# Kernel tuning notes

Measured on AMD Instinct MI355X. Metric: run time of the kernel, lower is better.

Reference implementation:

```python
import jax, jax.numpy as jnp
import numpy as np

NUM_TOURS = 200   # fixed segment count (original: tour_index.max()+1)
EPS = 1e-5        # torch InstanceNorm1d default eps


def setup_inputs() -> dict:
    key = jax.random.key(0)
    ks = jax.random.split(key, 9)
    B, P, D = 64, 2000, 128
    embeddings = jax.random.normal(ks[0], (B, P + 1, D), jnp.float32)
    tour_index = jax.random.randint(ks[1], (B, P), 0, NUM_TOURS, dtype=jnp.int32)
    # tour_combiner: Linear(2D -> D); feedforward: Linear(D -> D); stored as (in, out)
    W1 = jax.random.normal(ks[2], (2 * D, D), jnp.float32) / np.sqrt(2 * D)
    b1 = jax.random.normal(ks[3], (D,), jnp.float32) * 0.01
    W2 = jax.random.normal(ks[4], (D, D), jnp.float32) / np.sqrt(D)
    b2 = jax.random.normal(ks[5], (D,), jnp.float32) * 0.01
    # InstanceNorm1d affine params (per channel)
    gamma = 1.0 + 0.1 * jax.random.normal(ks[6], (D,), jnp.float32)
    beta = 0.1 * jax.random.normal(ks[7], (D,), jnp.float32)
    return {
        "batch_size": B, "num_customers": P,
        "tour_index": tour_index, "embeddings": embeddings,
        "W1": W1, "b1": b1, "W2": W2, "b2": b2,
        "gamma": gamma, "beta": beta,
    }


def reference(batch_size, num_customers, tour_index, embeddings, W1, b1, W2, b2, gamma, beta):
    B, P = batch_size, num_customers
    D = embeddings.shape[-1]
    cust = embeddings[:, 1:]                                  # (B, P, D)
    # tour-level segment sum (scatter_add over tour ids, per batch)
    flat_idx = (tour_index + jnp.arange(B, dtype=tour_index.dtype)[:, None] * NUM_TOURS).reshape(-1)
    tour_emb = jax.ops.segment_sum(cust.reshape(B * P, D), flat_idx,
                                   num_segments=B * NUM_TOURS).reshape(B, NUM_TOURS, D)
    # gather tour embedding back to each customer
    cust_tour = jnp.take_along_axis(tour_emb, tour_index[:, :, None], axis=1)  # (B, P, D)
    # concat -> linear -> relu -> linear
    combined = jnp.concatenate([cust, cust_tour], axis=-1)    # (B, P, 2D)
    h = jax.nn.relu(combined @ W1 + b1)
    h = h @ W2 + b2
    # residual + instance norm over the customer axis, per channel
    added = cust + h
    mean = jnp.mean(added, axis=1, keepdims=True)
    var = jnp.var(added, axis=1, keepdims=True)
    normed = (added - mean) * jax.lax.rsqrt(var + EPS) * gamma + beta
    return jnp.concatenate([embeddings[:, :1], normed], axis=1)
```

## Files before the change

kernel.cpp:

```cpp
#include <hip/hip_runtime.h>
#include <stdint.h>

typedef unsigned short u16;
typedef __attribute__((ext_vector_type(8))) short short8;
typedef __attribute__((ext_vector_type(4))) float floatx4;

constexpr int B_ = 64, P_ = 2000, D_ = 128, T_ = 200;

__device__ __forceinline__ u16 f2bf(float f) {
  union { float f; uint32_t u; } v; v.f = f;
  return (u16)((v.u + 0x7fffu + ((v.u >> 16) & 1u)) >> 16);
}

__global__ __launch_bounds__(256) void k_pre(
    const int* __restrict__ tidx, int* __restrict__ list,
    int* __restrict__ goff, int* __restrict__ gcnt,
    const float* __restrict__ W1, const float* __restrict__ W2,
    u16* __restrict__ w1f, u16* __restrict__ w2f, float* __restrict__ ssum) {
  __shared__ int tix[P_];
  __shared__ int cnt[256], scan[256], cur[256];
  const int bid = blockIdx.x, tid = threadIdx.x;

  if (bid >= 64) {
    if (bid < 128) {
      ssum[(bid - 64) * 256 + tid] = 0.f;
      return;
    }
    int t = (bid - 128) * 256 + tid;
    if (t >= 6144) return;
    const float* W = (t < 4096) ? W1 : W2;
    u16* dst = (t < 4096) ? w1f : w2f;
    int fid = (t < 4096) ? t : t - 4096;
    int lane = fid & 63;
    int nt = (fid >> 6) & 7;
    int ks = fid >> 9;
    int quad = lane >> 4, c = lane & 15;
    int k0 = ks * 32 + quad * 8;
#pragma unroll
    for (int j = 0; j < 8; ++j)
      dst[(size_t)fid * 8 + j] = f2bf(W[(k0 + j) * D_ + nt * 16 + c]);
    return;
  }

  const int b = bid;
  cnt[tid] = 0;
  for (int i = tid; i < P_; i += 256) tix[i] = tidx[b * P_ + i];
  __syncthreads();
  for (int i = tid; i < P_; i += 256) atomicAdd(&cnt[tix[i]], 1);
  __syncthreads();
  scan[tid] = cnt[tid];
  __syncthreads();
  for (int s = 1; s < 256; s <<= 1) {
    int v = (tid >= s) ? scan[tid - s] : 0;
    __syncthreads();
    scan[tid] += v;
    __syncthreads();
  }
  int excl = scan[tid] - cnt[tid];
  if (tid < T_) {
    goff[b * T_ + tid] = excl;
    gcnt[b * T_ + tid] = cnt[tid];
  }
  cur[tid] = excl;
  __syncthreads();
  for (int i = tid; i < P_; i += 256) {
    int slot = atomicAdd(&cur[tix[i]], 1);
    list[b * P_ + slot] = i;
  }
}

__global__ __launch_bounds__(256) void k_gather(const float* __restrict__ emb,
                                                const int* __restrict__ list,
                                                const int* __restrict__ goff,
                                                const int* __restrict__ gcnt,
                                                u16* __restrict__ tourb) {
  const int tid = threadIdx.x;
  const int lane = tid & 63, wv = tid >> 6;
  const int seg = blockIdx.x * 4 + wv;
  const int b = seg / T_;
  const int off = goff[seg], cn = gcnt[seg];
  const int* lstb = list + b * P_;
  const float* eb = emb + ((size_t)(b * 2001 + 1)) * D_ + lane * 2;
  float sx = 0.f, sy = 0.f;
  for (int i = 0; i < cn; i += 8) {
    int pr[8];
#pragma unroll
    for (int j = 0; j < 8; ++j)
      if (i + j < cn) pr[j] = lstb[off + i + j];
    float2 v[8];
#pragma unroll
    for (int j = 0; j < 8; ++j)
      if (i + j < cn) v[j] = *(const float2*)(eb + (size_t)pr[j] * D_);
#pragma unroll
    for (int j = 0; j < 8; ++j)
      if (i + j < cn) { sx += v[j].x; sy += v[j].y; }
  }
  uint32_t pk = (uint32_t)f2bf(sx) | ((uint32_t)f2bf(sy) << 16);
  ((uint32_t*)(tourb + (size_t)seg * D_))[lane] = pk;
}

__global__ __launch_bounds__(256, 8) void k_mlp(
    const int* __restrict__ tidx, const float* __restrict__ emb,
    const u16* __restrict__ tourb,
    const u16* __restrict__ w1f, const u16* __restrict__ w2f,
    const float* __restrict__ b1, const float* __restrict__ b2,
    float* __restrict__ ssum, float* __restrict__ ssq,
    float* __restrict__ out) {
  __shared__ u16 hbuf[32 * 136];
  __shared__ float red[2][2][128];
  const int tid = threadIdx.x;
  const int w = tid >> 6, lane = tid & 63, quad = lane >> 4, c = lane & 15;
  const int wr = w >> 1, wc = w & 1;
  const int base = blockIdx.x * 32;
  const int r0 = wr * 16;

  for (int i = tid; i < 512; i += 256) ((float*)red)[i] = 0.f;

  const int blo = base / P_;
  const int bhi = (base + 31) / P_;
  const bool straddle = (blo != bhi);
  const int bsplit = bhi * P_;

  const int m0 = base + r0 + c;
  const int ab = m0 / P_, ap = m0 - ab * P_;
  const float* arow = emb + ((size_t)(ab * 2001 + 1 + ap)) * D_;
  const u16* trow = tourb + ((size_t)(ab * T_ + tidx[m0])) * D_;

  float bias1[4], bias2[4];
#pragma unroll
  for (int ntl = 0; ntl < 4; ++ntl) {
    bias1[ntl] = b1[(wc * 4 + ntl) * 16 + c];
    bias2[ntl] = b2[(wc * 4 + ntl) * 16 + c];
  }

  floatx4 acc[4];
#pragma unroll
  for (int ntl = 0; ntl < 4; ++ntl) acc[ntl] = (floatx4)0.f;

#pragma unroll
  for (int ks = 0; ks < 8; ++ks) {
    short8 a;
    if (ks < 4) {
      const float* src = arow + ks * 32 + quad * 8;
      floatx4 x0 = *(const floatx4*)src;
      floatx4 x1 = *(const floatx4*)(src + 4);
#pragma unroll
      for (int j = 0; j < 4; ++j) {
        a[j]     = (short)f2bf(x0[j]);
        a[4 + j] = (short)f2bf(x1[j]);
      }
    } else {
      a = *(const short8*)(trow + (ks - 4) * 32 + quad * 8);
    }
#pragma unroll
    for (int ntl = 0; ntl < 4; ++ntl) {
      int nt = wc * 4 + ntl;
      short8 bf = *(const short8*)(w1f + ((size_t)((ks * 8 + nt) * 64 + lane)) * 8);
      acc[ntl] = __builtin_amdgcn_mfma_f32_16x16x32_bf16(a, bf, acc[ntl], 0, 0, 0);
    }
  }

#pragma unroll
  for (int ntl = 0; ntl < 4; ++ntl)
#pragma unroll
    for (int r = 0; r < 4; ++r) {
      int row = r0 + quad * 4 + r;
      float v = acc[ntl][r] + bias1[ntl];
      hbuf[row * 136 + wc * 64 + ntl * 16 + c] = f2bf(v > 0.f ? v : 0.f);
    }
  __syncthreads();

  floatx4 acc2[4];
#pragma unroll
  for (int ntl = 0; ntl < 4; ++ntl) acc2[ntl] = (floatx4)0.f;

#pragma unroll
  for (int ks = 0; ks < 4; ++ks) {
    short8 a = *(const short8*)(&hbuf[(r0 + c) * 136 + ks * 32 + quad * 8]);
#pragma unroll
    for (int ntl = 0; ntl < 4; ++ntl) {
      int nt = wc * 4 + ntl;
      short8 bf = *(const short8*)(w2f + ((size_t)((ks * 8 + nt) * 64 + lane)) * 8);
      acc2[ntl] = __builtin_amdgcn_mfma_f32_16x16x32_bf16(a, bf, acc2[ntl], 0, 0, 0);
    }
  }

  float s[4], q[4];
#pragma unroll
  for (int ntl = 0; ntl < 4; ++ntl) { s[ntl] = 0.f; q[ntl] = 0.f; }
#pragma unroll
  for (int ntl = 0; ntl < 4; ++ntl)
#pragma unroll
    for (int r = 0; r < 4; ++r) {
      int row = r0 + quad * 4 + r;
      int m = base + row;
      int b = m / P_, p = m - b * P_;
      int col = wc * 64 + ntl * 16 + c;
      size_t gaddr = ((size_t)(b * 2001 + 1 + p)) * D_ + col;
      float v = emb[gaddr] + (acc2[ntl][r] + bias2[ntl]);
      out[gaddr] = v;
      if (!straddle || m < bsplit) {
        s[ntl] += v; q[ntl] += v * v;
      } else {
        atomicAdd(&red[1][0][col], v);
        atomicAdd(&red[1][1][col], v * v);
      }
    }
#pragma unroll
  for (int ntl = 0; ntl < 4; ++ntl) {
    s[ntl] += __shfl_xor(s[ntl], 16);
    s[ntl] += __shfl_xor(s[ntl], 32);
    q[ntl] += __shfl_xor(q[ntl], 16);
    q[ntl] += __shfl_xor(q[ntl], 32);
  }
  if (quad == 0) {
#pragma unroll
    for (int ntl = 0; ntl < 4; ++ntl) {
      int col = wc * 64 + ntl * 16 + c;
      atomicAdd(&red[0][0][col], s[ntl]);
      atomicAdd(&red[0][1][col], q[ntl]);
    }
  }
  __syncthreads();
  if (tid < 128) {
    atomicAdd(&ssum[blo * D_ + tid], red[0][0][tid]);
    if (straddle) atomicAdd(&ssum[bhi * D_ + tid], red[1][0][tid]);
  } else {
    int col = tid - 128;
    atomicAdd(&ssq[blo * D_ + col], red[0][1][col]);
    if (straddle) atomicAdd(&ssq[bhi * D_ + col], red[1][1][col]);
  }
}

__global__ __launch_bounds__(256) void k_out(
    const float* __restrict__ emb,
    const float* __restrict__ ssum, const float* __restrict__ ssq,
    const float* __restrict__ gamma, const float* __restrict__ beta,
    float* __restrict__ out) {
  size_t i = ((size_t)blockIdx.x * 256 + threadIdx.x) * 8;
  int row = (int)(i >> 7), col = (int)(i & 127);
  int b = row / 2001, r = row - b * 2001;
  if (r == 0) {
    *(floatx4*)(out + i)     = *(const floatx4*)(emb + i);
    *(floatx4*)(out + i + 4) = *(const floatx4*)(emb + i + 4);
  } else {
    floatx4 a0 = *(const floatx4*)(out + i);
    floatx4 a1 = *(const floatx4*)(out + i + 4);
    int cc = b * D_ + col;
    floatx4 su0 = *(const floatx4*)(ssum + cc);
    floatx4 su1 = *(const floatx4*)(ssum + cc + 4);
    floatx4 sq0 = *(const floatx4*)(ssq + cc);
    floatx4 sq1 = *(const floatx4*)(ssq + cc + 4);
    floatx4 g0  = *(const floatx4*)(gamma + col);
    floatx4 g1  = *(const floatx4*)(gamma + col + 4);
    floatx4 be0 = *(const floatx4*)(beta + col);
    floatx4 be1 = *(const floatx4*)(beta + col + 4);
    constexpr float invP = 1.f / P_;
#pragma unroll
    for (int j = 0; j < 4; ++j) {
      float mean = su0[j] * invP;
      float var  = sq0[j] * invP - mean * mean;
      float sc   = rsqrtf(var + 1e-5f) * g0[j];
      a0[j] = a0[j] * sc + (be0[j] - mean * sc);
      float mean1 = su1[j] * invP;
      float var1  = sq1[j] * invP - mean1 * mean1;
      float sc1   = rsqrtf(var1 + 1e-5f) * g1[j];
      a1[j] = a1[j] * sc1 + (be1[j] - mean1 * sc1);
    }
    *(floatx4*)(out + i)     = a0;
    *(floatx4*)(out + i + 4) = a1;
  }
}

extern "C" void kernel_launch(void* const* d_in, const int* in_sizes, int n_in,
                              void* d_out, int out_size, void* d_ws, size_t ws_size,
                              hipStream_t stream) {
  const int*   tour_index = (const int*)d_in[2];
  const float* emb   = (const float*)d_in[3];
  const float* W1    = (const float*)d_in[4];
  const float* b1    = (const float*)d_in[5];
  const float* W2    = (const float*)d_in[6];
  const float* b2    = (const float*)d_in[7];
  const float* gamma = (const float*)d_in[8];
  const float* beta  = (const float*)d_in[9];
  float* out = (float*)d_out;
  char* ws = (char*)d_ws;

  u16*   w1f   = (u16*)(ws);
  u16*   w2f   = (u16*)(ws + 65536);
  float* ssum  = (float*)(ws + 98304);
  float* ssq   = ssum + B_ * D_;
  u16*   tourb = (u16*)(ws + 229376);
  int*   list  = (int*)(ws + 3506176);
  int*   goff  = (int*)(ws + 4018176);
  int*   gcnt  = (int*)(ws + 4069376);

  hipLaunchKernelGGL(k_pre,    dim3(152),  dim3(256), 0, stream,
                     tour_index, list, goff, gcnt, W1, W2, w1f, w2f, ssum);
  hipLaunchKernelGGL(k_gather, dim3(3200), dim3(256), 0, stream, emb, list, goff, gcnt, tourb);
  hipLaunchKernelGGL(k_mlp,    dim3(4000), dim3(256), 0, stream, tour_index, emb, tourb,
                     w1f, w2f, b1, b2, ssum, ssq, out);
  hipLaunchKernelGGL(k_out,    dim3(8004), dim3(256), 0, stream, emb, ssum, ssq, gamma, beta, out);
}
```

Baseline: 222.3 us.

## Stage MLP weights through double-buffered LDS with async global-to-LDS loads

Weight tiles for both GEMMs are no longer read directly from global memory by every wave. They are streamed into a double-buffered shared-memory tile with global_load_lds, prefetching the next k-slice while the current one feeds the MFMAs. Activation and tour rows, plus the residual embedding values, are now loaded early into registers so their latency overlaps compute. This adds a barrier per k-step and more LDS and register use, and the occupancy hint drops from 8 to 5 blocks.

```diff
diff --git a/kernel.cpp b/kernel.cpp
--- a/kernel.cpp
+++ b/kernel.cpp
@@ -10,6 +10,12 @@
 __device__ __forceinline__ u16 f2bf(float f) {
   union { float f; uint32_t u; } v; v.f = f;
   return (u16)((v.u + 0x7fffu + ((v.u >> 16) & 1u)) >> 16);
+}
+
+__device__ __forceinline__ void g2lds16(const void* g, void* l) {
+  __builtin_amdgcn_global_load_lds(
+      (const __attribute__((address_space(1))) uint32_t*)g,
+      (__attribute__((address_space(3))) uint32_t*)l, 16, 0, 0);
 }
 
 __global__ __launch_bounds__(256) void k_pre(
@@ -99,13 +105,14 @@
   ((uint32_t*)(tourb + (size_t)seg * D_))[lane] = pk;
 }
 
-__global__ __launch_bounds__(256, 8) void k_mlp(
+__global__ __launch_bounds__(256, 5) void k_mlp(
     const int* __restrict__ tidx, const float* __restrict__ emb,
     const u16* __restrict__ tourb,
     const u16* __restrict__ w1f, const u16* __restrict__ w2f,
     const float* __restrict__ b1, const float* __restrict__ b2,
     float* __restrict__ ssum, float* __restrict__ ssq,
     float* __restrict__ out) {
+  __shared__ u16 wbuf[2][4096];
   __shared__ u16 hbuf[32 * 136];
   __shared__ float red[2][2][128];
   const int tid = threadIdx.x;
@@ -126,6 +133,21 @@
   const float* arow = emb + ((size_t)(ab * 2001 + 1 + ap)) * D_;
   const u16* trow = tourb + ((size_t)(ab * T_ + tidx[m0])) * D_;
 
+  g2lds16(w1f + (size_t)tid * 8,        (u16*)wbuf[0] + (size_t)tid * 8);
+  g2lds16(w1f + 2048 + (size_t)tid * 8, (u16*)wbuf[0] + 2048 + (size_t)tid * 8);
+
+  floatx4 xa[4][2];
+#pragma unroll
+  for (int ks = 0; ks < 4; ++ks) {
+    const float* src = arow + ks * 32 + quad * 8;
+    xa[ks][0] = *(const floatx4*)src;
+    xa[ks][1] = *(const floatx4*)(src + 4);
+  }
+  short8 ta[4];
+#pragma unroll
+  for (int ks = 0; ks < 4; ++ks)
+    ta[ks] = *(const short8*)(trow + ks * 32 + quad * 8);
+
   float bias1[4], bias2[4];
 #pragma unroll
   for (int ntl = 0; ntl < 4; ++ntl) {
@@ -137,38 +159,56 @@
 #pragma unroll
   for (int ntl = 0; ntl < 4; ++ntl) acc[ntl] = (floatx4)0.f;
 
+  __syncthreads();
+
 #pragma unroll
   for (int ks = 0; ks < 8; ++ks) {
+    const int cur = ks & 1;
+    if (ks < 7) {
+      const u16* src = w1f + (size_t)(ks + 1) * 4096;
+      g2lds16(src + (size_t)tid * 8,        (u16*)wbuf[cur ^ 1] + (size_t)tid * 8);
+      g2lds16(src + 2048 + (size_t)tid * 8, (u16*)wbuf[cur ^ 1] + 2048 + (size_t)tid * 8);
+    } else {
+      g2lds16(w2f + (size_t)tid * 8,        (u16*)wbuf[0] + (size_t)tid * 8);
+      g2lds16(w2f + 2048 + (size_t)tid * 8, (u16*)wbuf[0] + 2048 + (size_t)tid * 8);
+    }
     short8 a;
     if (ks < 4) {
-      const float* src = arow + ks * 32 + quad * 8;
-      floatx4 x0 = *(const floatx4*)src;
-      floatx4 x1 = *(const floatx4*)(src + 4);
 #pragma unroll
       for (int j = 0; j < 4; ++j) {
-        a[j]     = (short)f2bf(x0[j]);
-        a[4 + j] = (short)f2bf(x1[j]);
+        a[j]     = (short)f2bf(xa[ks][0][j]);
+        a[4 + j] = (short)f2bf(xa[ks][1][j]);
       }
     } else {
-      a = *(const short8*)(trow + (ks - 4) * 32 + quad * 8);
+      a = ta[ks - 4];
     }
 #pragma unroll
     for (int ntl = 0; ntl < 4; ++ntl) {
-      int nt = wc * 4 + ntl;
-      short8 bf = *(const short8*)(w1f + ((size_t)((ks * 8 + nt) * 64 + lane)) * 8);
+      short8 bf = *(const short8*)(&wbuf[cur][((wc * 4 + ntl) * 64 + lane) * 8]);
       acc[ntl] = __builtin_amdgcn_mfma_f32_16x16x32_bf16(a, bf, acc[ntl], 0, 0, 0);
     }
-  }
-
+    if (ks == 7) {
+#pragma unroll
+      for (int ntl = 0; ntl < 4; ++ntl)
+#pragma unroll
+        for (int r = 0; r < 4; ++r) {
+          int row = r0 + quad * 4 + r;
+          float v = acc[ntl][r] + bias1[ntl];
+          hbuf[row * 136 + wc * 64 + ntl * 16 + c] = f2bf(v > 0.f ? v : 0.f);
+        }
+    }
+    __syncthreads();
+  }
+
+  float eemb[4][4];
 #pragma unroll
   for (int ntl = 0; ntl < 4; ++ntl)
 #pragma unroll
     for (int r = 0; r < 4; ++r) {
-      int row = r0 + quad * 4 + r;
-      float v = acc[ntl][r] + bias1[ntl];
-      hbuf[row * 136 + wc * 64 + ntl * 16 + c] = f2bf(v > 0.f ? v : 0.f);
-    }
-  __syncthreads();
+      int m = base + r0 + quad * 4 + r;
+      int b = m / P_, p = m - b * P_;
+      eemb[ntl][r] = emb[((size_t)(b * 2001 + 1 + p)) * D_ + wc * 64 + ntl * 16 + c];
+    }
 
   floatx4 acc2[4];
 #pragma unroll
@@ -176,13 +216,19 @@
 
 #pragma unroll
   for (int ks = 0; ks < 4; ++ks) {
+    const int cur = ks & 1;
+    if (ks < 3) {
+      const u16* src = w2f + (size_t)(ks + 1) * 4096;
+      g2lds16(src + (size_t)tid * 8,        (u16*)wbuf[cur ^ 1] + (size_t)tid * 8);
+      g2lds16(src + 2048 + (size_t)tid * 8, (u16*)wbuf[cur ^ 1] + 2048 + (size_t)tid * 8);
+    }
     short8 a = *(const short8*)(&hbuf[(r0 + c) * 136 + ks * 32 + quad * 8]);
 #pragma unroll
     for (int ntl = 0; ntl < 4; ++ntl) {
-      int nt = wc * 4 + ntl;
-      short8 bf = *(const short8*)(w2f + ((size_t)((ks * 8 + nt) * 64 + lane)) * 8);
+      short8 bf = *(const short8*)(&wbuf[cur][((wc * 4 + ntl) * 64 + lane) * 8]);
       acc2[ntl] = __builtin_amdgcn_mfma_f32_16x16x32_bf16(a, bf, acc2[ntl], 0, 0, 0);
     }
+    if (ks < 3) __syncthreads();
   }
 
   float s[4], q[4];
@@ -197,7 +243,7 @@
       int b = m / P_, p = m - b * P_;
       int col = wc * 64 + ntl * 16 + c;
       size_t gaddr = ((size_t)(b * 2001 + 1 + p)) * D_ + col;
-      float v = emb[gaddr] + (acc2[ntl][r] + bias2[ntl]);
+      float v = eemb[ntl][r] + (acc2[ntl][r] + bias2[ntl]);
       out[gaddr] = v;
       if (!straddle || m < bsplit) {
         s[ntl] += v; q[ntl] += v * v;
```

Result: faster. 210.9 us (-5.1%).
